# Kernel optimization log

Measured on AMD Instinct MI355X. Metric: run time of the kernel, lower is better.

Reference implementation:

```python
import jax, jax.numpy as jnp
import numpy as np

# Module constants derived from default grid_config
D = 59          # depth bins: (60-1)/1
C_OUT = 64
X, Y, Z = 128, 128, 7
STRIDE = 16
GRID_LB = np.array([-51.2, -51.2, -2.5], dtype=np.float32)
GRID_IV = np.array([0.8, 0.8, 1.0], dtype=np.float32)
D0, DSTEP = 1.0, 1.0

B, N, C_IN, H, W = 4, 6, 256, 16, 44


def _voxel_coords():
    xs, ys, zs = np.meshgrid(np.arange(X), np.arange(Y), np.arange(Z), indexing='ij')
    coords = np.stack([xs, ys, zs], axis=-1).reshape(-1, 3).astype(np.float32)
    coords = coords * GRID_IV + GRID_LB  # [V, 3] ego-frame voxel centers
    return coords


def _camera_rig(rng):
    """Realistic 6-camera rig: yawed cameras looking outward, z_cam = forward."""
    c2e = np.zeros((B, N, 4, 4), dtype=np.float32)
    K = np.zeros((B, N, 3, 3), dtype=np.float32)
    for b in range(B):
        for n in range(N):
            a = 2.0 * np.pi * n / N + 0.02 * rng.standard_normal()
            f = np.array([np.cos(a), np.sin(a), 0.0])           # camera forward (z_cam)
            x_cam = np.array([-np.sin(a), np.cos(a), 0.0])      # camera right
            y_cam = np.array([0.0, 0.0, -1.0])                   # camera down
            R = np.stack([x_cam, y_cam, f], axis=1)              # columns = cam axes in ego
            t = 1.0 * f + np.array([0.0, 0.0, 1.5])
            c2e[b, n, :3, :3] = R
            c2e[b, n, :3, 3] = t
            c2e[b, n, 3, 3] = 1.0
            fl = 400.0 + 5.0 * rng.standard_normal()
            K[b, n] = np.array([[fl, 0.0, 352.0], [0.0, fl, 128.0], [0.0, 0.0, 1.0]])
    return c2e, K


def setup_inputs() -> dict:
    key = jax.random.key(0)
    k1, k2, k3 = jax.random.split(key, 3)
    img_feats = jax.random.normal(k1, (B, N, C_IN, H, W), dtype=jnp.float32)
    c2e, K = _camera_rig(np.random.default_rng(0))
    # depth_net: 1x1 conv in_channels -> D + C_OUT
    w_depth = jax.random.normal(k2, (D + C_OUT, C_IN), dtype=jnp.float32) * (1.0 / np.sqrt(C_IN))
    b_depth = jax.random.normal(k3, (D + C_OUT,), dtype=jnp.float32) * 0.01
    return {
        'img_feats': img_feats,
        'cam2ego': jnp.asarray(c2e),
        'cam_intrinsics': jnp.asarray(K),
        'w_depth': w_depth,
        'b_depth': b_depth,
    }


def reference(img_feats, cam2ego, cam_intrinsics, w_depth, b_depth):
    Bc, Nc, C, Hc, Wc = img_feats.shape
    # 1x1 conv == per-pixel linear
    x = jnp.einsum('bnchw,oc->bnhwo', img_feats, w_depth) + b_depth  # [B,N,H,W,D+C_OUT]
    depth = jax.nn.softmax(x[..., :D], axis=-1)                      # [B,N,H,W,D]
    feat = x[..., D:]                                                # [B,N,H,W,C_OUT]

    vox = jnp.asarray(_voxel_coords())                               # [V,3]
    V = vox.shape[0]
    vox_h = jnp.concatenate([vox, jnp.ones((V, 1), vox.dtype)], axis=1)  # [V,4]

    e2c = jnp.linalg.inv(cam2ego)                                    # [B,N,4,4]
    cam = jnp.einsum('bnij,vj->bnvi', e2c, vox_h)[..., :3]           # [B,N,V,3]
    z = cam[..., 2]
    z_safe = jnp.maximum(z, 0.1)
    norm = cam[..., :2] / z_safe[..., None]
    homo = jnp.concatenate([norm, jnp.ones_like(z[..., None])], axis=-1)  # [B,N,V,3]
    img = jnp.einsum('bnij,bnvj->bnvi', cam_intrinsics, homo)[..., :2]
    fc = img / STRIDE                                                # feature-plane coords

    depth_bin = ((z - D0) / DSTEP).astype(jnp.int32)                 # trunc toward 0, matches .long()
    valid = (
        (fc[..., 0] >= 0) & (fc[..., 0] < Wc)
        & (fc[..., 1] >= 0) & (fc[..., 1] < Hc)
        & (z > 0.5)
        & (depth_bin >= 0) & (depth_bin < D)
    )

    u = jnp.clip(fc[..., 0].astype(jnp.int32), 0, Wc - 1)            # [B,N,V]
    v = jnp.clip(fc[..., 1].astype(jnp.int32), 0, Hc - 1)
    d = jnp.clip(depth_bin, 0, D - 1)
    hw = v * Wc + u

    feat_flat = feat.reshape(Bc, Nc, Hc * Wc, C_OUT)
    sampled_feat = jnp.take_along_axis(feat_flat, hw[..., None], axis=2)   # [B,N,V,C_OUT]
    depth_flat = depth.reshape(Bc, Nc, Hc * Wc * D)
    sampled_depth = jnp.take_along_axis(depth_flat, hw * D + d, axis=2)    # [B,N,V]

    wgt = sampled_depth * valid.astype(sampled_depth.dtype)
    # scatter_add at flat_idx == voxel index (identity) -> masked sum over cameras
    bev = jnp.einsum('bnv,bnvc->bvc', wgt, sampled_feat)             # [B,V,C_OUT]
    bev = bev.reshape(Bc, X, Y, Z, C_OUT).sum(axis=3)                # collapse Z
    bev = bev.transpose(0, 3, 2, 1)                                  # [B,C_OUT,Y,X]
    return bev, depth
```

## Files before the change

### kernel.cpp

```cpp
#include <hip/hip_runtime.h>
#include <math.h>

#define D_BINS 59
#define CO     64
#define CI     256
#define NB     4
#define NC     6
#define H_IMG  16
#define W_IMG  44
#define HW     704
#define NPIX   (NB*NC*HW)
#define XD     128
#define YD     128
#define ZD     7
#define NOUT   123

typedef float v2f __attribute__((ext_vector_type(2)));

__device__ void inv_rigid(const float* __restrict__ M, float* __restrict__ o) {
    double a = M[0], b = M[1], c = M[2], t0 = M[3];
    double d = M[4], e = M[5], f = M[6], t1 = M[7];
    double g = M[8], h = M[9], ii = M[10], t2 = M[11];
    double A00 = e*ii - f*h, A01 = c*h - b*ii, A02 = b*f - c*e;
    double A10 = f*g - d*ii, A11 = a*ii - c*g, A12 = c*d - a*f;
    double A20 = d*h - e*g,  A21 = b*g - a*h,  A22 = a*e - b*d;
    double det = a*A00 + b*A10 + c*A20;
    double inv = 1.0 / det;
    double r00 = A00*inv, r01 = A01*inv, r02 = A02*inv;
    double r10 = A10*inv, r11 = A11*inv, r12 = A12*inv;
    double r20 = A20*inv, r21 = A21*inv, r22 = A22*inv;
    o[0] = (float)r00; o[1] = (float)r01; o[2]  = (float)r02;
    o[3] = (float)(-(r00*t0 + r01*t1 + r02*t2));
    o[4] = (float)r10; o[5] = (float)r11; o[6]  = (float)r12;
    o[7] = (float)(-(r10*t0 + r11*t1 + r12*t2));
    o[8] = (float)r20; o[9] = (float)r21; o[10] = (float)r22;
    o[11] = (float)(-(r20*t0 + r21*t1 + r22*t2));
}

__global__ __launch_bounds__(256) void k_pre(
    const float* __restrict__ wd, float* __restrict__ wt2) {
    const int o = blockIdx.x;
    const int k = threadIdx.x;
    float v = (o < NOUT) ? wd[(size_t)o * CI + k] : 0.f;
    wt2[(size_t)(k >> 1) * 256 + o * 2 + (k & 1)] = v;
}

__global__ __launch_bounds__(1024, 8) void k_head(
    const float* __restrict__ img, const float* __restrict__ wt2,
    const float* __restrict__ bd, float* __restrict__ depth_out,
    float* __restrict__ feat_ws) {
    __shared__ float smem[64 * 132 + 64];
    float* S = smem + 64 * 132;

    const int tid = threadIdx.x;
    const int wv  = tid >> 6;
    const int ln  = tid & 63;
    const int p0  = blockIdx.x * 64;
    const int bn  = p0 / HW;
    const int hw0 = p0 - bn * HW;
    const int o0  = __builtin_amdgcn_readfirstlane(wv << 3);

    const float* imgb = img + (size_t)bn * CI * HW + hw0;

    v2f acc[8];
#pragma unroll
    for (int j = 0; j < 8; ++j) acc[j] = (v2f)(0.f);

    for (int kc = 0; kc < 4; ++kc) {
#pragma unroll
        for (int it = 0; it < 4; ++it) {
            int i = tid + it * 1024;
            int kl = i >> 6, px = i & 63;
            smem[(kl >> 1) * 130 + px * 2 + (kl & 1)] =
                imgb[(size_t)(kc * 64 + kl) * HW + px];
        }
        __syncthreads();
#pragma unroll 4
        for (int k2 = 0; k2 < 32; ++k2) {
            v2f a = *(const v2f*)(smem + k2 * 130 + ln * 2);
            const v2f* w =
                (const v2f*)(wt2 + (size_t)(kc * 32 + k2) * 256) + o0;
#pragma unroll
            for (int j = 0; j < 8; ++j)
                acc[j] = __builtin_elementwise_fma(a, w[j], acc[j]);
        }
        __syncthreads();
    }

    float* X = smem;
#pragma unroll
    for (int j = 0; j < 8; ++j) {
        int o = o0 + j;
        if (o < NOUT) {
            int col = (o < D_BINS) ? o : o + 5;
            X[ln * 132 + col] = (acc[j].x + acc[j].y) + bd[o];
        }
    }
    __syncthreads();

    {
        int p = tid >> 4, m = tid & 15;
        float4 v = *(const float4*)(X + p * 132 + 64 + m * 4);
        *(float4*)(feat_ws + (size_t)(p0 + p) * CO + m * 4) = v;
    }

    if (tid < 64) {
        float* row = X + tid * 132;
        float m = row[0];
        for (int o = 1; o < D_BINS; ++o) m = fmaxf(m, row[o]);
        float s = 0.f;
        for (int o = 0; o < D_BINS; ++o) {
            float e = __expf(row[o] - m);
            row[o] = e;
            s += e;
        }
        S[tid] = 1.f / s;
    }
    __syncthreads();

    for (int g = tid; g < 64 * D_BINS; g += 1024) {
        int p = g / D_BINS;
        int o = g - p * D_BINS;
        depth_out[(size_t)p0 * D_BINS + g] = X[p * 132 + o] * S[p];
    }
}

__global__ __launch_bounds__(256) void k_splat(
    const float* __restrict__ c2e, const float* __restrict__ Kmat,
    const float* __restrict__ depth_g, const float* __restrict__ feat_ws,
    float* __restrict__ bev) {
    __shared__ int   hw_s[ZD][64];
    __shared__ float wgt_s[ZD][64];
    __shared__ float E_s[NC][12];

    const int tx = threadIdx.x;
    const int cq = threadIdx.y;
    const int x = blockIdx.x * 64 + tx;
    const int y = blockIdx.y;
    const int b = blockIdx.z;

    if (cq == 0 && tx < NC)
        inv_rigid(c2e + (size_t)(b * NC + tx) * 16, &E_s[tx][0]);
    __syncthreads();

    const float wx = (float)x * 0.8f + (-51.2f);
    const float wy = (float)y * 0.8f + (-51.2f);

    float acc[16];
#pragma unroll
    for (int m = 0; m < 16; ++m) acc[m] = 0.f;

    for (int n = 0; n < NC; ++n) {
        const int bn = b * NC + n;
        const float* E = &E_s[n][0];
        const float* Km = Kmat + bn * 9;
        const float k00 = Km[0], k01 = Km[1], k02 = Km[2];
        const float k10 = Km[3], k11 = Km[4], k12 = Km[5];
        const float e02 = E[2], e12 = E[6], e22 = E[10];
        const float bx0 = E[0] * wx + E[1] * wy + E[3];
        const float bx1 = E[4] * wx + E[5] * wy + E[7];
        const float bx2 = E[8] * wx + E[9] * wy + E[11];

#pragma unroll
        for (int zz = 0; zz < 2; ++zz) {
            const int z = cq + zz * 4;
            if (z < ZD) {
                const float wz = -2.5f + (float)z;
                const float cx = bx0 + e02 * wz;
                const float cy = bx1 + e12 * wz;
                const float cz = bx2 + e22 * wz;
                const float zs = fmaxf(cz, 0.1f);
                const float rz = 1.0f / zs;
                const float xn = cx * rz;
                const float yn = cy * rz;
                const float fu = (k00 * xn + k01 * yn + k02) * 0.0625f;
                const float fv = (k10 * xn + k11 * yn + k12) * 0.0625f;
                const int bin = (int)(cz - 1.0f);
                const bool valid = (fu >= 0.f) & (fu < (float)W_IMG) &
                                   (fv >= 0.f) & (fv < (float)H_IMG) &
                                   (cz > 0.5f) & (bin >= 0) & (bin < D_BINS);
                int hw = -1;
                float wgt = 0.f;
                if (valid) {
                    int u = (int)fu;
                    int v = (int)fv;
                    hw = v * W_IMG + u;
                    wgt = depth_g[((size_t)bn * HW + hw) * D_BINS + bin];
                }
                hw_s[z][tx] = hw;
                wgt_s[z][tx] = wgt;
            }
        }
        __syncthreads();

#pragma unroll
        for (int z = 0; z < ZD; ++z) {
            const int hw = hw_s[z][tx];
            if (hw >= 0) {
                const float wgt = wgt_s[z][tx];
                const float4* fp =
                    (const float4*)(feat_ws + ((size_t)bn * HW + hw) * CO + cq * 16);
                float4 f0 = fp[0], f1 = fp[1], f2 = fp[2], f3 = fp[3];
                acc[0]  = fmaf(wgt, f0.x, acc[0]);
                acc[1]  = fmaf(wgt, f0.y, acc[1]);
                acc[2]  = fmaf(wgt, f0.z, acc[2]);
                acc[3]  = fmaf(wgt, f0.w, acc[3]);
                acc[4]  = fmaf(wgt, f1.x, acc[4]);
                acc[5]  = fmaf(wgt, f1.y, acc[5]);
                acc[6]  = fmaf(wgt, f1.z, acc[6]);
                acc[7]  = fmaf(wgt, f1.w, acc[7]);
                acc[8]  = fmaf(wgt, f2.x, acc[8]);
                acc[9]  = fmaf(wgt, f2.y, acc[9]);
                acc[10] = fmaf(wgt, f2.z, acc[10]);
                acc[11] = fmaf(wgt, f2.w, acc[11]);
                acc[12] = fmaf(wgt, f3.x, acc[12]);
                acc[13] = fmaf(wgt, f3.y, acc[13]);
                acc[14] = fmaf(wgt, f3.z, acc[14]);
                acc[15] = fmaf(wgt, f3.w, acc[15]);
            }
        }
        __syncthreads();
    }
    float* ob = bev + (((size_t)b * CO + cq * 16) * YD + y) * XD + x;
#pragma unroll
    for (int m = 0; m < 16; ++m) ob[(size_t)m * YD * XD] = acc[m];
}

extern "C" void kernel_launch(void* const* d_in, const int* in_sizes, int n_in,
                              void* d_out, int out_size, void* d_ws, size_t ws_size,
                              hipStream_t stream) {
    const float* img  = (const float*)d_in[0];
    const float* c2e  = (const float*)d_in[1];
    const float* Kmat = (const float*)d_in[2];
    const float* wd   = (const float*)d_in[3];
    const float* bd   = (const float*)d_in[4];
    float* bev = (float*)d_out;
    float* depth_out = bev + (size_t)NB * CO * YD * XD;
    float* feat_ws = (float*)d_ws;
    float* wt2 = feat_ws + (size_t)NPIX * CO;

    k_pre<<<128, 256, 0, stream>>>(wd, wt2);
    k_head<<<NPIX / 64, 1024, 0, stream>>>(img, wt2, bd, depth_out, feat_ws);
    k_splat<<<dim3(2, YD, NB), dim3(64, 4, 1), 0, stream>>>(c2e, Kmat, depth_out,
                                                            feat_ws, bev);
}
```

Measured before the change: 132.3 us.

## Split depth-head output channels across two blocks and precompute camera inverses

The 1x1-conv head kernel now runs two 512-thread blocks per 64-pixel tile, each computing half of the output channels. This doubles the number of blocks so more CUs can be kept busy. The cost is that each image tile is read twice, and feature stores become scalar and strided rather than float4. The rigid-transform inversion moves from every splat block into the weight-prep kernel and is written to workspace once, so splat blocks no longer do the inversion or the extra barrier.

```diff
diff --git a/kernel.cpp b/kernel.cpp
--- a/kernel.cpp
+++ b/kernel.cpp
@@ -38,19 +38,22 @@
 }
 
 __global__ __launch_bounds__(256) void k_pre(
-    const float* __restrict__ wd, float* __restrict__ wt2) {
+    const float* __restrict__ wd, const float* __restrict__ c2e,
+    float* __restrict__ wt2, float* __restrict__ e2c) {
     const int o = blockIdx.x;
     const int k = threadIdx.x;
     float v = (o < NOUT) ? wd[(size_t)o * CI + k] : 0.f;
     wt2[(size_t)(k >> 1) * 256 + o * 2 + (k & 1)] = v;
-}
-
-__global__ __launch_bounds__(1024, 8) void k_head(
+    if (blockIdx.x == 0 && k < NB * NC)
+        inv_rigid(c2e + k * 16, e2c + k * 12);
+}
+
+__global__ __launch_bounds__(512, 4) void k_head(
     const float* __restrict__ img, const float* __restrict__ wt2,
     const float* __restrict__ bd, float* __restrict__ depth_out,
     float* __restrict__ feat_ws) {
-    __shared__ float smem[64 * 132 + 64];
-    float* S = smem + 64 * 132;
+    __shared__ float smem[64 * 69 + 64];
+    float* S = smem + 64 * 69;
 
     const int tid = threadIdx.x;
     const int wv  = tid >> 6;
@@ -58,7 +61,8 @@
     const int p0  = blockIdx.x * 64;
     const int bn  = p0 / HW;
     const int hw0 = p0 - bn * HW;
-    const int o0  = __builtin_amdgcn_readfirstlane(wv << 3);
+    const int ob  = blockIdx.y << 6;
+    const int o0  = __builtin_amdgcn_readfirstlane(ob + (wv << 3));
 
     const float* imgb = img + (size_t)bn * CI * HW + hw0;
 
@@ -68,8 +72,8 @@
 
     for (int kc = 0; kc < 4; ++kc) {
 #pragma unroll
-        for (int it = 0; it < 4; ++it) {
-            int i = tid + it * 1024;
+        for (int it = 0; it < 8; ++it) {
+            int i = tid + it * 512;
             int kl = i >> 6, px = i & 63;
             smem[(kl >> 1) * 130 + px * 2 + (kl & 1)] =
                 imgb[(size_t)(kc * 64 + kl) * HW + px];
@@ -91,58 +95,55 @@
 #pragma unroll
     for (int j = 0; j < 8; ++j) {
         int o = o0 + j;
-        if (o < NOUT) {
-            int col = (o < D_BINS) ? o : o + 5;
-            X[ln * 132 + col] = (acc[j].x + acc[j].y) + bd[o];
-        }
+        if (o < NOUT)
+            X[ln * 69 + (o - ob)] = (acc[j].x + acc[j].y) + bd[o];
     }
     __syncthreads();
 
-    {
-        int p = tid >> 4, m = tid & 15;
-        float4 v = *(const float4*)(X + p * 132 + 64 + m * 4);
-        *(float4*)(feat_ws + (size_t)(p0 + p) * CO + m * 4) = v;
-    }
-
-    if (tid < 64) {
-        float* row = X + tid * 132;
-        float m = row[0];
-        for (int o = 1; o < D_BINS; ++o) m = fmaxf(m, row[o]);
-        float s = 0.f;
-        for (int o = 0; o < D_BINS; ++o) {
-            float e = __expf(row[o] - m);
-            row[o] = e;
-            s += e;
-        }
-        S[tid] = 1.f / s;
-    }
-    __syncthreads();
-
-    for (int g = tid; g < 64 * D_BINS; g += 1024) {
-        int p = g / D_BINS;
-        int o = g - p * D_BINS;
-        depth_out[(size_t)p0 * D_BINS + g] = X[p * 132 + o] * S[p];
+    if (ob == 0) {
+        if (tid < 320) {
+            int p = tid / 5, c = tid - p * 5;
+            feat_ws[(size_t)(p0 + p) * CO + c] = X[p * 69 + 59 + c];
+        }
+        if (tid < 64) {
+            float* row = X + tid * 69;
+            float m = row[0];
+            for (int o = 1; o < D_BINS; ++o) m = fmaxf(m, row[o]);
+            float s = 0.f;
+            for (int o = 0; o < D_BINS; ++o) {
+                float e = __expf(row[o] - m);
+                row[o] = e;
+                s += e;
+            }
+            S[tid] = 1.f / s;
+        }
+        __syncthreads();
+        for (int g = tid; g < 64 * D_BINS; g += 512) {
+            int p = g / D_BINS;
+            int o = g - p * D_BINS;
+            depth_out[(size_t)p0 * D_BINS + g] = X[p * 69 + o] * S[p];
+        }
+    } else {
+        for (int g = tid; g < 64 * D_BINS; g += 512) {
+            int p = g / D_BINS;
+            int j = g - p * D_BINS;
+            feat_ws[(size_t)(p0 + p) * CO + 5 + j] = X[p * 69 + j];
+        }
     }
 }
 
 __global__ __launch_bounds__(256) void k_splat(
-    const float* __restrict__ c2e, const float* __restrict__ Kmat,
+    const float* __restrict__ e2c, const float* __restrict__ Kmat,
     const float* __restrict__ depth_g, const float* __restrict__ feat_ws,
     float* __restrict__ bev) {
     __shared__ int   hw_s[ZD][64];
     __shared__ float wgt_s[ZD][64];
-    __shared__ float E_s[NC][12];
 
     const int tx = threadIdx.x;
     const int cq = threadIdx.y;
     const int x = blockIdx.x * 64 + tx;
     const int y = blockIdx.y;
     const int b = blockIdx.z;
-
-    if (cq == 0 && tx < NC)
-        inv_rigid(c2e + (size_t)(b * NC + tx) * 16, &E_s[tx][0]);
-    __syncthreads();
-
     const float wx = (float)x * 0.8f + (-51.2f);
     const float wy = (float)y * 0.8f + (-51.2f);
 
@@ -152,7 +153,7 @@
 
     for (int n = 0; n < NC; ++n) {
         const int bn = b * NC + n;
-        const float* E = &E_s[n][0];
+        const float* E = e2c + bn * 12;
         const float* Km = Kmat + bn * 9;
         const float k00 = Km[0], k01 = Km[1], k02 = Km[2];
         const float k10 = Km[3], k11 = Km[4], k12 = Km[5];
@@ -238,9 +239,10 @@
     float* depth_out = bev + (size_t)NB * CO * YD * XD;
     float* feat_ws = (float*)d_ws;
     float* wt2 = feat_ws + (size_t)NPIX * CO;
-
-    k_pre<<<128, 256, 0, stream>>>(wd, wt2);
-    k_head<<<NPIX / 64, 1024, 0, stream>>>(img, wt2, bd, depth_out, feat_ws);
-    k_splat<<<dim3(2, YD, NB), dim3(64, 4, 1), 0, stream>>>(c2e, Kmat, depth_out,
+    float* e2c = wt2 + 128 * 256;
+
+    k_pre<<<128, 256, 0, stream>>>(wd, c2e, wt2, e2c);
+    k_head<<<dim3(NPIX / 64, 2), 512, 0, stream>>>(img, wt2, bd, depth_out, feat_ws);
+    k_splat<<<dim3(2, YD, NB), dim3(64, 4, 1), 0, stream>>>(e2c, Kmat, depth_out,
                                                             feat_ws, bev);
 }
```

Result: faster. 127.3 us (-3.8%).
